# Kernel optimization log

Hardware: AMD Instinct MI355X
Metric: run time of the kernel (lower is better)

Reference implementation:

```python
import jax, jax.numpy as jnp
import numpy as np

B, H, D, M = 128, 8, 256, 8192
K, RANK = 32, 16
EPS = 1e-8


def setup_inputs() -> dict:
    key = jax.random.key(0)
    ks = jax.random.split(key, 8)
    s = 0.02
    inv_sqrt_d = 1.0 / np.sqrt(D).astype(np.float32)
    return {
        "psi": jax.random.normal(ks[0], (B, D, 2), jnp.float32),
        "u_real": jax.random.normal(ks[1], (M, D), jnp.float32) * s,
        "u_imag": jax.random.normal(ks[2], (M, D), jnp.float32) * s,
        "w_real": jax.random.normal(ks[3], (M, D), jnp.float32) * s,
        "w_imag": jax.random.normal(ks[4], (M, D), jnp.float32) * s,
        "s_logit": jnp.full((M,), -2.0, jnp.float32),
        # orthogonal init approximated by scaled gaussian (init only, not math)
        "probe_real": jax.random.normal(ks[5], (H, D, D), jnp.float32) * inv_sqrt_d,
        "probe_imag": jax.random.normal(ks[6], (H, D, D), jnp.float32) * inv_sqrt_d,
        "k": K,
        "rank": RANK,
    }


def reference(psi, u_real, u_imag, w_real, w_imag, s_logit,
              probe_real, probe_imag, k, rank):
    temperature = 1.0
    # ---- project_query: q_h = (Wr + i Wi) psi,  psi: [B,d,2] -> q: [B,H,d] complex parts
    pr, pi = psi[..., 0], psi[..., 1]
    qr = jnp.einsum('hij,bj->bhi', probe_real, pr) - jnp.einsum('hij,bj->bhi', probe_imag, pi)
    qi = jnp.einsum('hij,bj->bhi', probe_real, pi) + jnp.einsum('hij,bj->bhi', probe_imag, pr)
    # ---- effect_directions: L2-normalize complex u over d
    nrm = jnp.sqrt(jnp.clip(jnp.sum(u_real**2 + u_imag**2, axis=-1, keepdims=True), EPS))
    ur, ui = u_real / nrm, u_imag / nrm
    # ---- probe scores: |u_m^dag q|^2 * sigma(s_m) / tau  -> [B,H,M]
    ip_r = jnp.einsum('md,bhd->bhm', ur, qr) + jnp.einsum('md,bhd->bhm', ui, qi)
    ip_i = jnp.einsum('md,bhd->bhm', ur, qi) - jnp.einsum('md,bhd->bhm', ui, qr)
    scores = jax.nn.sigmoid(s_logit)[None, None, :] * (ip_r**2 + ip_i**2) / max(temperature, 1e-6)
    # ---- top-k select + gather directions/values, weight by sqrt(score)
    topk_vals, topk_idx = jax.lax.top_k(scores, k)          # [B,H,k]
    u_c = (ur + 1j * ui).astype(jnp.complex64)[topk_idx]    # [B,H,k,d]
    w_c = (w_real + 1j * w_imag).astype(jnp.complex64)[topk_idx]
    weights = jnp.sqrt(jnp.clip(topk_vals, 0.0))[..., None] # [B,H,k,1]
    u_mat = jnp.swapaxes(u_c * weights, -1, -2)             # [B,H,d,k]
    w_mat = jnp.swapaxes(w_c * weights, -1, -2)             # [B,H,d,k]
    # ---- batched complex QR, pad/truncate Q to rank cols
    Q, _ = jnp.linalg.qr(u_mat)                             # [B,H,d,min(d,k)]
    cols = Q.shape[-1]
    if cols < rank:
        Q = jnp.concatenate([Q, jnp.zeros(Q.shape[:-1] + (rank - cols,), Q.dtype)], axis=-1)
    elif cols > rank:
        Q = Q[..., :rank]
    # ---- align values: V = Q[:, :eff] * diag(Q^H w)
    coeff = jnp.einsum('bhdr,bhdk->bhrk', Q.conj(), w_c.swapaxes(-1, -2) * 0 + w_mat)  # [B,H,rank,k]
    eff = min(rank, k)
    diag = jnp.diagonal(coeff[..., :eff, :eff], axis1=-2, axis2=-1)  # [B,H,eff]
    V = Q[..., :eff] * diag[..., None, :]
    if eff < rank:
        V = jnp.concatenate([V, jnp.zeros(V.shape[:-1] + (rank - eff,), V.dtype)], axis=-1)
    U_re = jnp.stack([Q.real, Q.imag], axis=-1)  # [B,H,d,rank,2]
    V_re = jnp.stack([V.real, V.imag], axis=-1)  # [B,H,d,rank,2]
    return (U_re, V_re)
```

## Files before the change

### kernel.cpp

```cpp
#include <hip/hip_runtime.h>
#include <math.h>

#define BB 128
#define HH 8
#define DD 256
#define MM 8192
#define BH (BB*HH)
#define RANK 16

typedef __attribute__((ext_vector_type(8))) short bf16x8;
typedef __attribute__((ext_vector_type(4))) float f32x4;

__device__ inline unsigned short f2bf(float f) {
  unsigned x = __float_as_uint(f);
  unsigned r = x + 0x7FFFu + ((x >> 16) & 1u);
  return (unsigned short)(r >> 16);
}
__device__ inline float bf2f(unsigned short u) {
  return __uint_as_float(((unsigned)u) << 16);
}

__global__ __launch_bounds__(256) void k_q(
    const float* __restrict__ psi, const float* __restrict__ probe_r,
    const float* __restrict__ probe_i, float* __restrict__ qr, float* __restrict__ qi) {
  __shared__ float2 ps0[DD];
  __shared__ float2 ps1[DD];
  int b0 = blockIdx.x * 2;
  int h  = blockIdx.y;
  int i  = threadIdx.x;
  ps0[i] = ((const float2*)psi)[(size_t)b0 * DD + i];
  ps1[i] = ((const float2*)psi)[(size_t)(b0 + 1) * DD + i];
  __syncthreads();
  const float* rr = probe_r + ((size_t)h * DD + i) * DD;
  const float* ri = probe_i + ((size_t)h * DD + i) * DD;
  float a0r = 0.f, a0i = 0.f, a1r = 0.f, a1i = 0.f;
  for (int j = 0; j < DD; j += 4) {
    float4 xr = *(const float4*)(rr + j);
    float4 xi = *(const float4*)(ri + j);
    float2 p0 = ps0[j+0], p1 = ps0[j+1], p2 = ps0[j+2], p3 = ps0[j+3];
    a0r += xr.x*p0.x - xi.x*p0.y;  a0i += xr.x*p0.y + xi.x*p0.x;
    a0r += xr.y*p1.x - xi.y*p1.y;  a0i += xr.y*p1.y + xi.y*p1.x;
    a0r += xr.z*p2.x - xi.z*p2.y;  a0i += xr.z*p2.y + xi.z*p2.x;
    a0r += xr.w*p3.x - xi.w*p3.y;  a0i += xr.w*p3.y + xi.w*p3.x;
    float2 s0 = ps1[j+0], s1 = ps1[j+1], s2 = ps1[j+2], s3 = ps1[j+3];
    a1r += xr.x*s0.x - xi.x*s0.y;  a1i += xr.x*s0.y + xi.x*s0.x;
    a1r += xr.y*s1.x - xi.y*s1.y;  a1i += xr.y*s1.y + xi.y*s1.x;
    a1r += xr.z*s2.x - xi.z*s2.y;  a1i += xr.z*s2.y + xi.z*s2.x;
    a1r += xr.w*s3.x - xi.w*s3.y;  a1i += xr.w*s3.y + xi.w*s3.x;
  }
  size_t o0 = ((size_t)(b0    ) * HH + h) * DD + i;
  size_t o1 = ((size_t)(b0 + 1) * HH + h) * DD + i;
  qr[o0] = a0r; qi[o0] = a0i;
  qr[o1] = a1r; qi[o1] = a1i;
}

__global__ __launch_bounds__(256) void k_norm(
    const float* __restrict__ u_r, const float* __restrict__ u_i,
    const float* __restrict__ s_logit, float* __restrict__ inv_nrm,
    float* __restrict__ fac) {
  int m = blockIdx.x * 4 + (threadIdx.x >> 6);
  int lane = threadIdx.x & 63;
  const float4* a = (const float4*)(u_r + (size_t)m * DD);
  const float4* b = (const float4*)(u_i + (size_t)m * DD);
  float4 x = a[lane], y = b[lane];
  float s = x.x*x.x + x.y*x.y + x.z*x.z + x.w*x.w
          + y.x*y.x + y.y*y.y + y.z*y.z + y.w*y.w;
  for (int off = 32; off; off >>= 1) s += __shfl_down(s, off);
  if (lane == 0) {
    float inv = 1.0f / sqrtf(fmaxf(s, 1e-8f));
    inv_nrm[m] = inv;
    float sig = 1.0f / (1.0f + expf(-s_logit[m]));
    fac[m] = sig * inv * inv;
  }
}

__global__ __launch_bounds__(256) void k_convA(
    const float* __restrict__ qr, const float* __restrict__ qi,
    unsigned short* __restrict__ Ap) {
  int bh = blockIdx.x, d = threadIdx.x;
  float xr = qr[(size_t)bh*DD + d], xi = qi[(size_t)bh*DD + d];
  unsigned short hr = f2bf(xr), hi_ = f2bf(xi);
  unsigned short* r0 = Ap + (size_t)(2*bh) * 512;
  unsigned short* r1 = r0 + 512;
  r0[d] = hr;  r0[256+d] = hi_;
  r1[d] = hi_; r1[256+d] = hr ^ 0x8000u;
}

__global__ __launch_bounds__(256) void k_convB(
    const float* __restrict__ u_r, const float* __restrict__ u_i,
    unsigned short* __restrict__ Bp) {
  int m = blockIdx.x, d = threadIdx.x;
  unsigned short* r = Bp + (size_t)m * 512;
  r[d]     = f2bf(u_r[(size_t)m*DD + d]);
  r[256+d] = f2bf(u_i[(size_t)m*DD + d]);
}

__global__ __launch_bounds__(256, 4) void k_gemm(
    const unsigned short* __restrict__ Ap,
    const unsigned short* __restrict__ Bp,
    const float* __restrict__ fac,
    unsigned short* __restrict__ sc) {
  __shared__ __align__(16) unsigned short SMEM[16384];
  unsigned short* As = SMEM;
  unsigned short* Bs = SMEM + 8192;
  int tid  = threadIdx.x;
  int lane = tid & 63, wid = tid >> 6;
  int wm = wid >> 1, wn = wid & 1;
  int a_row0 = blockIdx.y * 128;
  int b_row0 = blockIdx.x * 128;

  int st_r0 = tid >> 3;
  int st_kc = tid & 7;
  int st_slot = (st_kc ^ (st_r0 & 7)) * 16;

  int arow = lane & 15;
  int fr_g = lane >> 4;
  int r7   = lane & 7;
  const char* Abase = (const char*)As + (wm*64 + arow) * 128;
  const char* Bbase = (const char*)Bs + (wn*64 + arow) * 128;

  f32x4 acc[4][4];
#pragma unroll
  for (int i = 0; i < 4; ++i)
#pragma unroll
    for (int j = 0; j < 4; ++j) acc[i][j] = (f32x4){0.f,0.f,0.f,0.f};

  int4 ra[4], rb[4];
  {
    const unsigned short* pa = Ap + (size_t)(a_row0 + st_r0)*512 + 8*st_kc;
    const unsigned short* pb = Bp + (size_t)(b_row0 + st_r0)*512 + 8*st_kc;
#pragma unroll
    for (int i = 0; i < 4; ++i) {
      ra[i] = *(const int4*)(pa + (size_t)i*32*512);
      rb[i] = *(const int4*)(pb + (size_t)i*32*512);
    }
  }
  const int NT = 8;
  for (int t = 0; t < NT; ++t) {
    __syncthreads();
#pragma unroll
    for (int i = 0; i < 4; ++i) {
      *(int4*)((char*)As + (st_r0 + 32*i)*128 + st_slot) = ra[i];
      *(int4*)((char*)Bs + (st_r0 + 32*i)*128 + st_slot) = rb[i];
    }
    __syncthreads();
    if (t + 1 < NT) {
      int k0 = (t + 1) * 64;
      const unsigned short* pa = Ap + (size_t)(a_row0 + st_r0)*512 + k0 + 8*st_kc;
      const unsigned short* pb = Bp + (size_t)(b_row0 + st_r0)*512 + k0 + 8*st_kc;
#pragma unroll
      for (int i = 0; i < 4; ++i) {
        ra[i] = *(const int4*)(pa + (size_t)i*32*512);
        rb[i] = *(const int4*)(pb + (size_t)i*32*512);
      }
    }
#pragma unroll
    for (int ks = 0; ks < 2; ++ks) {
      int slot = ((ks*4 + fr_g) ^ r7) * 16;
      bf16x8 a[4], b[4];
#pragma unroll
      for (int fm = 0; fm < 4; ++fm) a[fm] = *(const bf16x8*)(Abase + fm*2048 + slot);
#pragma unroll
      for (int fn = 0; fn < 4; ++fn) b[fn] = *(const bf16x8*)(Bbase + fn*2048 + slot);
#pragma unroll
      for (int fm = 0; fm < 4; ++fm)
#pragma unroll
        for (int fn = 0; fn < 4; ++fn)
          acc[fm][fn] = __builtin_amdgcn_mfma_f32_16x16x32_bf16(a[fm], b[fn], acc[fm][fn], 0, 0, 0);
    }
  }
  __syncthreads();
  const int LP = 136;
  int lr0 = wm*32 + 2*(lane >> 4);
  int lc0 = wn*64 + (lane & 15);
  float fv[4];
#pragma unroll
  for (int fn = 0; fn < 4; ++fn)
    fv[fn] = fac[blockIdx.x*128 + lc0 + fn*16];
#pragma unroll
  for (int fm = 0; fm < 4; ++fm) {
#pragma unroll
    for (int fn = 0; fn < 4; ++fn) {
      f32x4 c = acc[fm][fn];
      float s0 = fv[fn]*(c.x*c.x + c.y*c.y);
      float s1 = fv[fn]*(c.z*c.z + c.w*c.w);
      SMEM[(lr0 + fm*8    ) * LP + lc0 + fn*16] = f2bf(s0);
      SMEM[(lr0 + fm*8 + 1) * LP + lc0 + fn*16] = f2bf(s1);
    }
  }
  __syncthreads();
  {
    int row = tid >> 2;
    int seg = tid & 3;
    unsigned short* dst = sc + (size_t)(blockIdx.y*64 + row) * MM
                             + blockIdx.x*128 + seg*32;
    const unsigned short* src = SMEM + row*LP + seg*32;
#pragma unroll
    for (int c4 = 0; c4 < 4; ++c4)
      *(int4*)(dst + c4*8) = *(const int4*)(src + c4*8);
  }
}

__global__ __launch_bounds__(256) void k_top32(
    const unsigned short* __restrict__ sc, int* __restrict__ cand) {
  __shared__ unsigned long long wtop[128];
  int bh = blockIdx.x, half = blockIdx.y;
  int tid = threadIdx.x, lane = tid & 63, w = tid >> 6;
  const unsigned short* row = sc + (size_t)bh * MM + half*4096;
  unsigned long long v[16];
#pragma unroll
  for (int j = 0; j < 16; ++j) {
    int idx = j*256 + tid;
    unsigned bits = ((unsigned)row[idx]) << 16;
    v[j] = (((unsigned long long)bits) << 32) | (unsigned)(4095 - idx);
  }
  for (int r = 0; r < 32; ++r) {
    unsigned long long bk = v[0]; int bj = 0;
#pragma unroll
    for (int j = 1; j < 16; ++j) if (v[j] > bk) { bk = v[j]; bj = j; }
    unsigned long long mx = bk;
    for (int off = 32; off; off >>= 1) {
      unsigned long long o = __shfl_xor(mx, off);
      if (o > mx) mx = o;
    }
    if (bk == mx && mx != 0ull) {
#pragma unroll
      for (int j = 0; j < 16; ++j) if (j == bj) v[j] = 0ull;
    }
    if (lane == 0) wtop[w*32 + r] = mx;
  }
  __syncthreads();
  if (w == 0) {
    unsigned long long a = wtop[lane], b = wtop[64 + lane];
    for (int r = 0; r < 32; ++r) {
      unsigned long long bk = (a > b) ? a : b;
      int which = (a > b) ? 0 : 1;
      unsigned long long mx = bk;
      for (int off = 32; off; off >>= 1) {
        unsigned long long o = __shfl_xor(mx, off);
        if (o > mx) mx = o;
      }
      if (bk == mx && mx != 0ull) { if (which == 0) a = 0ull; else b = 0ull; }
      if (lane == 0) {
        int idx = 4095 - (int)(mx & 0xFFFFFFFFull);
        cand[bh*64 + half*32 + r] = half*4096 + idx;
      }
    }
  }
}

__global__ __launch_bounds__(256) void k_exact(
    const float* __restrict__ qr, const float* __restrict__ qi,
    const float* __restrict__ u_r, const float* __restrict__ u_i,
    const float* __restrict__ fac, const int* __restrict__ cand,
    float* __restrict__ topv, int* __restrict__ topi) {
  __shared__ float qrs[DD], qis[DD];
  __shared__ unsigned long long keys[64];
  int bh = blockIdx.x, tid = threadIdx.x, lane = tid & 63, w = tid >> 6;
  qrs[tid] = qr[(size_t)bh*DD + tid];
  qis[tid] = qi[(size_t)bh*DD + tid];
  __syncthreads();
  float4 xr = *(const float4*)&qrs[lane*4];
  float4 xi = *(const float4*)&qis[lane*4];
  for (int c = 0; c < 16; ++c) {
    int ci = w*16 + c;
    int m = cand[bh*64 + ci];
    float4 a = *(const float4*)(u_r + (size_t)m*DD + lane*4);
    float4 b = *(const float4*)(u_i + (size_t)m*DD + lane*4);
    float pr = a.x*xr.x + a.y*xr.y + a.z*xr.z + a.w*xr.w
             + b.x*xi.x + b.y*xi.y + b.z*xi.z + b.w*xi.w;
    float pi2 = a.x*xi.x + a.y*xi.y + a.z*xi.z + a.w*xi.w
              - (b.x*xr.x + b.y*xr.y + b.z*xr.z + b.w*xr.w);
    for (int off = 32; off; off >>= 1) {
      pr  += __shfl_down(pr, off);
      pi2 += __shfl_down(pi2, off);
    }
    if (lane == 0) {
      float s = fac[m] * (pr*pr + pi2*pi2);
      keys[ci] = (((unsigned long long)__float_as_uint(s)) << 32)
               | (unsigned)(MM - 1 - m);
    }
  }
  __syncthreads();
  if (w == 0) {
    unsigned long long k = keys[lane];
    for (int r = 0; r < 16; ++r) {
      unsigned long long mx = k;
      for (int off = 32; off; off >>= 1) {
        unsigned long long o = __shfl_xor(mx, off);
        if (o > mx) mx = o;
      }
      if (k == mx && mx != 0ull) k = 0ull;
      if (lane == 0) {
        topv[bh*16 + r] = __uint_as_float((unsigned)(mx >> 32));
        topi[bh*16 + r] = MM - 1 - (int)(mx & 0xFFFFFFFFull);
      }
    }
  }
}

__global__ __launch_bounds__(256) void k_qr(
    const float* __restrict__ u_r, const float* __restrict__ u_i,
    const float* __restrict__ inv_nrm,
    const float* __restrict__ w_r, const float* __restrict__ w_i,
    const float* __restrict__ topv, const int* __restrict__ topi,
    float* __restrict__ out) {
  __shared__ float redS[4];
  __shared__ float alphaSh[2];
  __shared__ float pw[4][32];
  __shared__ float tauSh[16][2];
  __shared__ int   idxs[16];
  __shared__ float fA[16], fW[16];

  int bh = blockIdx.x;
  int tid = threadIdx.x;
  int d = tid;
  int lane = tid & 63, wv = tid >> 6;

  if (tid < 16) {
    int id = topi[bh*16 + tid];
    idxs[tid] = id;
    float w = sqrtf(fmaxf(topv[bh*16 + tid], 0.f));
    fW[tid] = w;
    fA[tid] = w * inv_nrm[id];
  }
  __syncthreads();

  float Ar[16], Ai[16];
#pragma unroll
  for (int j = 0; j < 16; ++j) {
    float f = fA[j];
    size_t base = (size_t)idxs[j] * DD + d;
    Ar[j] = u_r[base] * f;
    Ai[j] = u_i[base] * f;
  }

  for (int j = 0; j < 16; ++j) {
    float ar = 0.f, ai = 0.f;
#pragma unroll
    for (int c = 0; c < 16; ++c) if (c == j) { ar = Ar[c]; ai = Ai[c]; }
    float xn2 = (d > j) ? (ar*ar + ai*ai) : 0.f;
    for (int off = 32; off; off >>= 1) xn2 += __shfl_down(xn2, off);
    if (lane == 0) redS[wv] = xn2;
    if (d == j) { alphaSh[0] = ar; alphaSh[1] = ai; }
    __syncthreads();
    xn2 = redS[0] + redS[1] + redS[2] + redS[3];
    float alr = alphaSh[0], ali = alphaSh[1];
    float taur, taui, scr, sci;
    if (xn2 == 0.f && ali == 0.f) {
      taur = 0.f; taui = 0.f; scr = 0.f; sci = 0.f;
    } else {
      float nrm  = sqrtf(alr*alr + ali*ali + xn2);
      float beta = (alr >= 0.f) ? -nrm : nrm;
      taur = (beta - alr) / beta;
      taui = -ali / beta;
      float dr = alr - beta, di = ali;
      float den = dr*dr + di*di;
      scr = dr / den; sci = -di / den;
    }
    if (tid == 0) { tauSh[j][0] = taur; tauSh[j][1] = taui; }
    float vr, vi;
    if (d > j)       { vr = ar*scr - ai*sci; vi = ar*sci + ai*scr; }
    else if (d == j) { vr = 1.f; vi = 0.f; }
    else             { vr = 0.f; vi = 0.f; }
#pragma unroll
    for (int c = 0; c < 16; ++c) if (c == j) { Ar[c] = vr; Ai[c] = vi; }
#pragma unroll
    for (int c = 0; c < 16; ++c) if (c > j) {
      float lr = vr*Ar[c] + vi*Ai[c];
      float li = vr*Ai[c] - vi*Ar[c];
      for (int off = 32; off; off >>= 1) {
        lr += __shfl_down(lr, off);
        li += __shfl_down(li, off);
      }
      if (lane == 0) { pw[wv][2*c] = lr; pw[wv][2*c+1] = li; }
    }
    __syncthreads();
    float tr = taur*vr + taui*vi;
    float ti = taur*vi - taui*vr;
#pragma unroll
    for (int c = 0; c < 16; ++c) if (c > j) {
      float wcr = pw[0][2*c] + pw[1][2*c] + pw[2][2*c] + pw[3][2*c];
      float wci = pw[0][2*c+1] + pw[1][2*c+1] + pw[2][2*c+1] + pw[3][2*c+1];
      Ar[c] -= tr*wcr - ti*wci;
      Ai[c] -= tr*wci + ti*wcr;
    }
  }

  for (int i = 15; i >= 0; --i) {
    __syncthreads();
    float taur = tauSh[i][0], taui = tauSh[i][1];
    float vr = 0.f, vi = 0.f;
#pragma unroll
    for (int c = 0; c < 16; ++c) if (c == i) { vr = Ar[c]; vi = Ai[c]; }
#pragma unroll
    for (int c = 0; c < 16; ++c) if (c > i) {
      float lr = vr*Ar[c] + vi*Ai[c];
      float li = vr*Ai[c] - vi*Ar[c];
      for (int off = 32; off; off >>= 1) {
        lr += __shfl_down(lr, off);
        li += __shfl_down(li, off);
      }
      if (lane == 0) { pw[wv][2*c] = lr; pw[wv][2*c+1] = li; }
    }
    __syncthreads();
    float tvr = taur*vr - taui*vi;
    float tvi = taur*vi + taui*vr;
#pragma unroll
    for (int c = 0; c < 16; ++c) if (c > i) {
      float wcr = pw[0][2*c] + pw[1][2*c] + pw[2][2*c] + pw[3][2*c];
      float wci = pw[0][2*c+1] + pw[1][2*c+1] + pw[2][2*c+1] + pw[3][2*c+1];
      Ar[c] -= tvr*wcr - tvi*wci;
      Ai[c] -= tvr*wci + tvi*wcr;
    }
    float er = (d == i) ? 1.f : 0.f;
#pragma unroll
    for (int c = 0; c < 16; ++c) if (c == i) { Ar[c] = er - tvr; Ai[c] = -tvi; }
  }

  __syncthreads();
#pragma unroll
  for (int r = 0; r < 16; ++r) {
    size_t base = (size_t)idxs[r] * DD + d;
    float wr2 = w_r[base], wi2 = w_i[base];
    float lr = Ar[r]*wr2 + Ai[r]*wi2;
    float li = Ar[r]*wi2 - Ai[r]*wr2;
    for (int off = 32; off; off >>= 1) {
      lr += __shfl_down(lr, off);
      li += __shfl_down(li, off);
    }
    if (lane == 0) { pw[wv][2*r] = lr; pw[wv][2*r+1] = li; }
  }
  __syncthreads();
  float dgR[16], dgI[16];
#pragma unroll
  for (int r = 0; r < 16; ++r) {
    float f = fW[r];
    dgR[r] = (pw[0][2*r] + pw[1][2*r] + pw[2][2*r] + pw[3][2*r]) * f;
    dgI[r] = (pw[0][2*r+1] + pw[1][2*r+1] + pw[2][2*r+1] + pw[3][2*r+1]) * f;
  }

  size_t baseU = ((size_t)bh * DD + d) * 32;
  size_t baseV = (size_t)BH * DD * 32 + baseU;
  float4* oU = (float4*)(out + baseU);
  float4* oV = (float4*)(out + baseV);
#pragma unroll
  for (int r = 0; r < 16; r += 2) {
    float q0r = Ar[r],   q0i = Ai[r];
    float q1r = Ar[r+1], q1i = Ai[r+1];
    oU[r >> 1] = make_float4(q0r, q0i, q1r, q1i);
    float v0r = q0r*dgR[r]   - q0i*dgI[r];
    float v0i = q0r*dgI[r]   + q0i*dgR[r];
    float v1r = q1r*dgR[r+1] - q1i*dgI[r+1];
    float v1i = q1r*dgI[r+1] + q1i*dgR[r+1];
    oV[r >> 1] = make_float4(v0r, v0i, v1r, v1i);
  }
}

extern "C" void kernel_launch(void* const* d_in, const int* in_sizes, int n_in,
                              void* d_out, int out_size, void* d_ws, size_t ws_size,
                              hipStream_t stream) {
  (void)in_sizes; (void)n_in; (void)out_size; (void)ws_size;
  const float* psi     = (const float*)d_in[0];
  const float* u_r     = (const float*)d_in[1];
  const float* u_i     = (const float*)d_in[2];
  const float* w_r     = (const float*)d_in[3];
  const float* w_i     = (const float*)d_in[4];
  const float* s_logit = (const float*)d_in[5];
  const float* probe_r = (const float*)d_in[6];
  const float* probe_i = (const float*)d_in[7];

  float* ws = (float*)d_ws;
  float*          qr      = ws;
  float*          qi      = ws + 262144;
  float*          inv_nrm = ws + 524288;
  float*          fac     = ws + 532480;
  float*          topv    = ws + 540672;
  int*            topi    = (int*)(ws + 557056);
  int*            cand    = (int*)(ws + 573440);
  unsigned short* Ap      = (unsigned short*)(ws + 638976);
  unsigned short* Bp      = (unsigned short*)(ws + 1163264);
  unsigned short* sc      = (unsigned short*)(ws + 3260416);
  float* out = (float*)d_out;

  hipLaunchKernelGGL(k_q,     dim3(BB/2, HH), dim3(256), 0, stream,
                     psi, probe_r, probe_i, qr, qi);
  hipLaunchKernelGGL(k_norm,  dim3(MM/4),     dim3(256), 0, stream,
                     u_r, u_i, s_logit, inv_nrm, fac);
  hipLaunchKernelGGL(k_convA, dim3(BH),       dim3(256), 0, stream, qr, qi, Ap);
  hipLaunchKernelGGL(k_convB, dim3(MM),       dim3(256), 0, stream, u_r, u_i, Bp);
  hipLaunchKernelGGL(k_gemm,  dim3(64, 16),   dim3(256), 0, stream,
                     Ap, Bp, fac, sc);
  hipLaunchKernelGGL(k_top32, dim3(BH, 2),    dim3(256), 0, stream, sc, cand);
  hipLaunchKernelGGL(k_exact, dim3(BH),       dim3(256), 0, stream,
                     qr, qi, u_r, u_i, fac, cand, topv, topi);
  hipLaunchKernelGGL(k_qr,    dim3(BH),       dim3(256), 0, stream,
                     u_r, u_i, inv_nrm, w_r, w_i, topv, topi, out);
}
```

Before: 551.7 us.

## Run Householder QR in a single wavefront per head to drop block barriers

```diff
diff --git a/kernel.cpp b/kernel.cpp
--- a/kernel.cpp
+++ b/kernel.cpp
@@ -299,53 +299,48 @@
   }
 }
 
-__global__ __launch_bounds__(256) void k_qr(
+__global__ __launch_bounds__(64) void k_qr(
     const float* __restrict__ u_r, const float* __restrict__ u_i,
     const float* __restrict__ inv_nrm,
     const float* __restrict__ w_r, const float* __restrict__ w_i,
     const float* __restrict__ topv, const int* __restrict__ topi,
     float* __restrict__ out) {
-  __shared__ float redS[4];
-  __shared__ float alphaSh[2];
-  __shared__ float pw[4][32];
-  __shared__ float tauSh[16][2];
-  __shared__ int   idxs[16];
-  __shared__ float fA[16], fW[16];
-
+  __shared__ float tauS[32];
   int bh = blockIdx.x;
-  int tid = threadIdx.x;
-  int d = tid;
-  int lane = tid & 63, wv = tid >> 6;
-
-  if (tid < 16) {
-    int id = topi[bh*16 + tid];
-    idxs[tid] = id;
-    float w = sqrtf(fmaxf(topv[bh*16 + tid], 0.f));
-    fW[tid] = w;
-    fA[tid] = w * inv_nrm[id];
-  }
-  __syncthreads();
-
-  float Ar[16], Ai[16];
+  int l  = threadIdx.x;
+
+  int   idxs[16];
+  float fW[16];
+  float Ar[4][16], Ai[4][16];
 #pragma unroll
   for (int j = 0; j < 16; ++j) {
-    float f = fA[j];
-    size_t base = (size_t)idxs[j] * DD + d;
-    Ar[j] = u_r[base] * f;
-    Ai[j] = u_i[base] * f;
+    int id = topi[bh*16 + j];
+    idxs[j] = id;
+    float wv = sqrtf(fmaxf(topv[bh*16 + j], 0.f));
+    fW[j] = wv;
+    float f = wv * inv_nrm[id];
+#pragma unroll
+    for (int k = 0; k < 4; ++k) {
+      size_t base = (size_t)id * DD + l + 64*k;
+      Ar[k][j] = u_r[base] * f;
+      Ai[k][j] = u_i[base] * f;
+    }
   }
 
   for (int j = 0; j < 16; ++j) {
-    float ar = 0.f, ai = 0.f;
-#pragma unroll
-    for (int c = 0; c < 16; ++c) if (c == j) { ar = Ar[c]; ai = Ai[c]; }
-    float xn2 = (d > j) ? (ar*ar + ai*ai) : 0.f;
-    for (int off = 32; off; off >>= 1) xn2 += __shfl_down(xn2, off);
-    if (lane == 0) redS[wv] = xn2;
-    if (d == j) { alphaSh[0] = ar; alphaSh[1] = ai; }
-    __syncthreads();
-    xn2 = redS[0] + redS[1] + redS[2] + redS[3];
-    float alr = alphaSh[0], ali = alphaSh[1];
+    float cAr[4], cAi[4];
+#pragma unroll
+    for (int c = 0; c < 16; ++c) if (c == j) {
+#pragma unroll
+      for (int k = 0; k < 4; ++k) { cAr[k] = Ar[k][c]; cAi[k] = Ai[k][c]; }
+    }
+    float xn2 = (l > j) ? (cAr[0]*cAr[0] + cAi[0]*cAi[0]) : 0.f;
+#pragma unroll
+    for (int k = 1; k < 4; ++k) xn2 += cAr[k]*cAr[k] + cAi[k]*cAi[k];
+#pragma unroll
+    for (int off = 32; off; off >>= 1) xn2 += __shfl_xor(xn2, off);
+    float alr = __shfl(cAr[0], j);
+    float ali = __shfl(cAi[0], j);
     float taur, taui, scr, sci;
     if (xn2 == 0.f && ali == 0.f) {
       taur = 0.f; taui = 0.f; scr = 0.f; sci = 0.f;
@@ -358,102 +353,131 @@
       float den = dr*dr + di*di;
       scr = dr / den; sci = -di / den;
     }
-    if (tid == 0) { tauSh[j][0] = taur; tauSh[j][1] = taui; }
-    float vr, vi;
-    if (d > j)       { vr = ar*scr - ai*sci; vi = ar*sci + ai*scr; }
-    else if (d == j) { vr = 1.f; vi = 0.f; }
-    else             { vr = 0.f; vi = 0.f; }
-#pragma unroll
-    for (int c = 0; c < 16; ++c) if (c == j) { Ar[c] = vr; Ai[c] = vi; }
-#pragma unroll
-    for (int c = 0; c < 16; ++c) if (c > j) {
-      float lr = vr*Ar[c] + vi*Ai[c];
-      float li = vr*Ai[c] - vi*Ar[c];
-      for (int off = 32; off; off >>= 1) {
-        lr += __shfl_down(lr, off);
-        li += __shfl_down(li, off);
-      }
-      if (lane == 0) { pw[wv][2*c] = lr; pw[wv][2*c+1] = li; }
-    }
-    __syncthreads();
-    float tr = taur*vr + taui*vi;
-    float ti = taur*vi - taui*vr;
-#pragma unroll
-    for (int c = 0; c < 16; ++c) if (c > j) {
-      float wcr = pw[0][2*c] + pw[1][2*c] + pw[2][2*c] + pw[3][2*c];
-      float wci = pw[0][2*c+1] + pw[1][2*c+1] + pw[2][2*c+1] + pw[3][2*c+1];
-      Ar[c] -= tr*wcr - ti*wci;
-      Ai[c] -= tr*wci + ti*wcr;
+    if (l == 0) { tauS[2*j] = taur; tauS[2*j+1] = taui; }
+    float vr[4], vi[4];
+    vr[0] = (l > j) ? (cAr[0]*scr - cAi[0]*sci) : ((l == j) ? 1.f : 0.f);
+    vi[0] = (l > j) ? (cAr[0]*sci + cAi[0]*scr) : 0.f;
+#pragma unroll
+    for (int k = 1; k < 4; ++k) {
+      vr[k] = cAr[k]*scr - cAi[k]*sci;
+      vi[k] = cAr[k]*sci + cAi[k]*scr;
+    }
+#pragma unroll
+    for (int c = 0; c < 16; ++c) if (c == j) {
+#pragma unroll
+      for (int k = 0; k < 4; ++k) { Ar[k][c] = vr[k]; Ai[k][c] = vi[k]; }
+    }
+    float pvr[4], pvi[4];
+#pragma unroll
+    for (int k = 0; k < 4; ++k) {
+      pvr[k] = taur*vr[k] + taui*vi[k];
+      pvi[k] = taur*vi[k] - taui*vr[k];
+    }
+#pragma unroll
+    for (int c = 0; c < 16; ++c) {
+      if (c > j) {
+        float lr = 0.f, li = 0.f;
+#pragma unroll
+        for (int k = 0; k < 4; ++k) {
+          lr += vr[k]*Ar[k][c] + vi[k]*Ai[k][c];
+          li += vr[k]*Ai[k][c] - vi[k]*Ar[k][c];
+        }
+#pragma unroll
+        for (int off = 32; off; off >>= 1) {
+          lr += __shfl_xor(lr, off);
+          li += __shfl_xor(li, off);
+        }
+#pragma unroll
+        for (int k = 0; k < 4; ++k) {
+          Ar[k][c] -= pvr[k]*lr - pvi[k]*li;
+          Ai[k][c] -= pvr[k]*li + pvi[k]*lr;
+        }
+      }
     }
   }
 
   for (int i = 15; i >= 0; --i) {
-    __syncthreads();
-    float taur = tauSh[i][0], taui = tauSh[i][1];
-    float vr = 0.f, vi = 0.f;
-#pragma unroll
-    for (int c = 0; c < 16; ++c) if (c == i) { vr = Ar[c]; vi = Ai[c]; }
-#pragma unroll
-    for (int c = 0; c < 16; ++c) if (c > i) {
-      float lr = vr*Ar[c] + vi*Ai[c];
-      float li = vr*Ai[c] - vi*Ar[c];
-      for (int off = 32; off; off >>= 1) {
-        lr += __shfl_down(lr, off);
-        li += __shfl_down(li, off);
-      }
-      if (lane == 0) { pw[wv][2*c] = lr; pw[wv][2*c+1] = li; }
-    }
-    __syncthreads();
-    float tvr = taur*vr - taui*vi;
-    float tvi = taur*vi + taui*vr;
-#pragma unroll
-    for (int c = 0; c < 16; ++c) if (c > i) {
-      float wcr = pw[0][2*c] + pw[1][2*c] + pw[2][2*c] + pw[3][2*c];
-      float wci = pw[0][2*c+1] + pw[1][2*c+1] + pw[2][2*c+1] + pw[3][2*c+1];
-      Ar[c] -= tvr*wcr - tvi*wci;
-      Ai[c] -= tvr*wci + tvi*wcr;
-    }
-    float er = (d == i) ? 1.f : 0.f;
-#pragma unroll
-    for (int c = 0; c < 16; ++c) if (c == i) { Ar[c] = er - tvr; Ai[c] = -tvi; }
-  }
-
-  __syncthreads();
+    float taur = tauS[2*i], taui = tauS[2*i+1];
+    float vr[4], vi[4];
+#pragma unroll
+    for (int c = 0; c < 16; ++c) if (c == i) {
+#pragma unroll
+      for (int k = 0; k < 4; ++k) { vr[k] = Ar[k][c]; vi[k] = Ai[k][c]; }
+    }
+    float pvr[4], pvi[4];
+#pragma unroll
+    for (int k = 0; k < 4; ++k) {
+      pvr[k] = taur*vr[k] - taui*vi[k];
+      pvi[k] = taur*vi[k] + taui*vr[k];
+    }
+#pragma unroll
+    for (int c = 0; c < 16; ++c) {
+      if (c > i) {
+        float lr = 0.f, li = 0.f;
+#pragma unroll
+        for (int k = 0; k < 4; ++k) {
+          lr += vr[k]*Ar[k][c] + vi[k]*Ai[k][c];
+          li += vr[k]*Ai[k][c] - vi[k]*Ar[k][c];
+        }
+#pragma unroll
+        for (int off = 32; off; off >>= 1) {
+          lr += __shfl_xor(lr, off);
+          li += __shfl_xor(li, off);
+        }
+#pragma unroll
+        for (int k = 0; k < 4; ++k) {
+          Ar[k][c] -= pvr[k]*lr - pvi[k]*li;
+          Ai[k][c] -= pvr[k]*li + pvi[k]*lr;
+        }
+      }
+    }
+    float er = (l == i) ? 1.f : 0.f;
+#pragma unroll
+    for (int c = 0; c < 16; ++c) if (c == i) {
+      Ar[0][c] = er - pvr[0];  Ai[0][c] = -pvi[0];
+#pragma unroll
+      for (int k = 1; k < 4; ++k) { Ar[k][c] = -pvr[k]; Ai[k][c] = -pvi[k]; }
+    }
+  }
+
+  float dgR[16], dgI[16];
 #pragma unroll
   for (int r = 0; r < 16; ++r) {
-    size_t base = (size_t)idxs[r] * DD + d;
-    float wr2 = w_r[base], wi2 = w_i[base];
-    float lr = Ar[r]*wr2 + Ai[r]*wi2;
-    float li = Ar[r]*wi2 - Ai[r]*wr2;
+    float lr = 0.f, li = 0.f;
+#pragma unroll
+    for (int k = 0; k < 4; ++k) {
+      size_t base = (size_t)idxs[r] * DD + l + 64*k;
+      float wr2 = w_r[base], wi2 = w_i[base];
+      lr += Ar[k][r]*wr2 + Ai[k][r]*wi2;
+      li += Ar[k][r]*wi2 - Ai[k][r]*wr2;
+    }
+#pragma unroll
     for (int off = 32; off; off >>= 1) {
-      lr += __shfl_down(lr, off);
-      li += __shfl_down(li, off);
-    }
-    if (lane == 0) { pw[wv][2*r] = lr; pw[wv][2*r+1] = li; }
-  }
-  __syncthreads();
-  float dgR[16], dgI[16];
-#pragma unroll
-  for (int r = 0; r < 16; ++r) {
-    float f = fW[r];
-    dgR[r] = (pw[0][2*r] + pw[1][2*r] + pw[2][2*r] + pw[3][2*r]) * f;
-    dgI[r] = (pw[0][2*r+1] + pw[1][2*r+1] + pw[2][2*r+1] + pw[3][2*r+1]) * f;
-  }
-
-  size_t baseU = ((size_t)bh * DD + d) * 32;
-  size_t baseV = (size_t)BH * DD * 32 + baseU;
-  float4* oU = (float4*)(out + baseU);
-  float4* oV = (float4*)(out + baseV);
-#pragma unroll
-  for (int r = 0; r < 16; r += 2) {
-    float q0r = Ar[r],   q0i = Ai[r];
-    float q1r = Ar[r+1], q1i = Ai[r+1];
-    oU[r >> 1] = make_float4(q0r, q0i, q1r, q1i);
-    float v0r = q0r*dgR[r]   - q0i*dgI[r];
-    float v0i = q0r*dgI[r]   + q0i*dgR[r];
-    float v1r = q1r*dgR[r+1] - q1i*dgI[r+1];
-    float v1i = q1r*dgI[r+1] + q1i*dgR[r+1];
-    oV[r >> 1] = make_float4(v0r, v0i, v1r, v1i);
+      lr += __shfl_xor(lr, off);
+      li += __shfl_xor(li, off);
+    }
+    dgR[r] = lr * fW[r];
+    dgI[r] = li * fW[r];
+  }
+
+#pragma unroll
+  for (int k = 0; k < 4; ++k) {
+    int d = l + 64*k;
+    size_t baseU = ((size_t)bh * DD + d) * 32;
+    size_t baseV = (size_t)BH * DD * 32 + baseU;
+    float4* oU = (float4*)(out + baseU);
+    float4* oV = (float4*)(out + baseV);
+#pragma unroll
+    for (int r = 0; r < 16; r += 2) {
+      float q0r = Ar[k][r],   q0i = Ai[k][r];
+      float q1r = Ar[k][r+1], q1i = Ai[k][r+1];
+      oU[r >> 1] = make_float4(q0r, q0i, q1r, q1i);
+      float v0r = q0r*dgR[r]   - q0i*dgI[r];
+      float v0i = q0r*dgI[r]   + q0i*dgR[r];
+      float v1r = q1r*dgR[r+1] - q1i*dgI[r+1];
+      float v1i = q1r*dgI[r+1] + q1i*dgR[r+1];
+      oV[r >> 1] = make_float4(v0r, v0i, v1r, v1i);
+    }
   }
 }
 
@@ -494,6 +518,6 @@
   hipLaunchKernelGGL(k_top32, dim3(BH, 2),    dim3(256), 0, stream, sc, cand);
   hipLaunchKernelGGL(k_exact, dim3(BH),       dim3(256), 0, stream,
                      qr, qi, u_r, u_i, fac, cand, topv, topi);
-  hipLaunchKernelGGL(k_qr,    dim3(BH),       dim3(256), 0, stream,
+  hipLaunchKernelGGL(k_qr,    dim3(BH),       dim3(64),  0, stream,
                      u_r, u_i, inv_nrm, w_r, w_i, topv, topi, out);
 }
```

Result: faster. 477.0 us (-13.5%).
